# Kernel tuning notes

Hardware: AMD Instinct MI355X
Metric: run time of the kernel (lower is better)

The kernel has to match this reference:

```python
import jax, jax.numpy as jnp
import numpy as np

N_IN, N_HID, N_OUT = 128, 128, 128
BATCH = 131072

def _linear_params(key, fan_in, fan_out):
    # torch nn.Linear default init: U(-1/sqrt(fan_in), 1/sqrt(fan_in))
    kw, kb = jax.random.split(key)
    bound = 1.0 / np.sqrt(fan_in)
    W = jax.random.uniform(kw, (fan_out, fan_in), jnp.float32, -bound, bound)
    b = jax.random.uniform(kb, (fan_out,), jnp.float32, -bound, bound)
    return W, b

def setup_inputs() -> dict:
    key = jax.random.key(0)
    ks = jax.random.split(key, 6)
    x = jax.random.normal(ks[0], (BATCH, N_IN), jnp.float32)
    hidden = jnp.zeros((BATCH, N_HID), jnp.float32)
    ctx = jnp.zeros((BATCH, N_HID), jnp.float32)
    Wf, bf = _linear_params(ks[1], N_IN + N_HID, N_HID)
    Wi, bi = _linear_params(ks[2], N_IN + N_HID, N_HID)
    Wc, bc = _linear_params(ks[3], N_IN + N_HID, N_HID)
    Wo, bo = _linear_params(ks[4], N_IN + N_HID, N_HID)
    Wfc, bfc = _linear_params(ks[5], N_HID, N_OUT)
    return {"x": x, "hidden": hidden, "ctx": ctx,
            "Wf": Wf, "bf": bf, "Wi": Wi, "bi": bi,
            "Wc": Wc, "bc": bc, "Wo": Wo, "bo": bo,
            "Wfc": Wfc, "bfc": bfc}

def reference(x, hidden, ctx, Wf, bf, Wi, bi, Wc, bc, Wo, bo, Wfc, bfc):
    # cat order matches torch: (hidden, x)
    cat_input = jnp.concatenate([hidden, x], axis=1)  # [B, n_hid+n_in]
    # Stack the four gate weights into one GEMM, then split (same math).
    W4 = jnp.concatenate([Wf, Wi, Wc, Wo], axis=0)    # [4*n_hid, n_hid+n_in]
    b4 = jnp.concatenate([bf, bi, bc, bo], axis=0)
    gates = cat_input @ W4.T + b4                     # [B, 4*n_hid]
    f_lin, i_lin, c_lin, o_lin = jnp.split(gates, 4, axis=1)
    f_t = jax.nn.sigmoid(f_lin)
    i_t = jax.nn.sigmoid(i_lin)
    c_t_temp = jnp.tanh(c_lin)
    ctx_new = f_t * ctx + i_t * c_t_temp
    o_t = jax.nn.sigmoid(o_lin)
    hidden_new = o_t * jnp.tanh(ctx_new)
    out = hidden_new @ Wfc.T + bfc                    # [B, n_out]
    return (out, hidden_new, ctx_new)
```

## Files before the change

### kernel.cpp

```cpp
#include <hip/hip_runtime.h>

#define BATCH   131072
#define NHID    128
#define KDIM    256
#define BM      32
#define TPB     512
#define NBLK    256
#define NTILE   (BATCH / BM)
#define TPBLK   (NTILE / NBLK)

typedef __bf16 bf16_t;
typedef __bf16 bf16x4 __attribute__((ext_vector_type(4)));
typedef __bf16 bf16x8 __attribute__((ext_vector_type(8)));
typedef float  f32x4  __attribute__((ext_vector_type(4)));

__device__ __forceinline__ float fsigmoid(float v) {
    return __builtin_amdgcn_rcpf(1.0f + __builtin_amdgcn_exp2f(v * -1.44269504f));
}
__device__ __forceinline__ float ftanh(float v) {
    return __builtin_fmaf(-2.0f,
        __builtin_amdgcn_rcpf(1.0f + __builtin_amdgcn_exp2f(v * 2.88539008f)), 1.0f);
}

__global__ void prep_kernel(const float* __restrict__ Wf, const float* __restrict__ Wi,
                            const float* __restrict__ Wc, const float* __restrict__ Wo,
                            const float* __restrict__ bfp, const float* __restrict__ bip,
                            const float* __restrict__ bcp, const float* __restrict__ bop,
                            const float* __restrict__ Wfc,
                            bf16_t* __restrict__ W4p, float* __restrict__ b4p,
                            bf16_t* __restrict__ Wfcb)
{
    int id = blockIdx.x * 256 + threadIdx.x;
    if (id < 512 * 256) {
        int p = id >> 8, k = id & 255;
        int w = p >> 6, t = (p >> 4) & 3, c = p & 15;
        int j = w * 16 + c;
        const float* W = (t == 0) ? Wf : (t == 1) ? Wi : (t == 2) ? Wc : Wo;
        W4p[id] = (bf16_t)W[j * 256 + k];
        if (k == 0) {
            const float* bs = (t == 0) ? bfp : (t == 1) ? bip : (t == 2) ? bcp : bop;
            b4p[p] = bs[j];
        }
    } else {
        int id2 = id - 512 * 256;
        if (id2 < 128 * 128) Wfcb[id2] = (bf16_t)Wfc[id2];
    }
}

__global__ __launch_bounds__(TPB, 2) void lstm_fused(
    const float* __restrict__ x, const float* __restrict__ hidden, const float* __restrict__ ctx,
    const bf16_t* __restrict__ W4p, const float* __restrict__ b4p,
    const bf16_t* __restrict__ Wfcb, const float* __restrict__ bfc,
    float* __restrict__ out, float* __restrict__ hid_out, float* __restrict__ ctx_out)
{
    __shared__ __align__(16) char lds[2 * 16384 + 2 * 8192];

    const int tid  = threadIdx.x;
    const int lane = tid & 63;
    const int wv   = tid >> 6;
    const int l16  = lane & 15;
    const int lq   = lane >> 4;
    const int jcol = wv * 16 + l16;
    const int tile0 = blockIdx.x * TPBLK;

    const int r_s = tid >> 4;
    const int c_s = tid & 15;
    const int swzS = (r_s & 7) << 4;
    const int swzA = (l16 & 7) << 4;

    bf16x8 B1[32];
    {
        const bf16_t* Bp = W4p + (wv * 64 + l16) * 256 + lq * 8;
        #pragma unroll
        for (int gt = 0; gt < 4; ++gt)
            #pragma unroll
            for (int ks = 0; ks < 8; ++ks)
                B1[gt * 8 + ks] = *(const bf16x8*)(Bp + gt * 16 * 256 + ks * 32);
    }
    bf16x8 b2r[4];
    {
        const bf16_t* B2 = Wfcb + jcol * 128 + lq * 8;
        #pragma unroll
        for (int ks = 0; ks < 4; ++ks) b2r[ks] = *(const bf16x8*)(B2 + ks * 32);
    }
    const float bfv = b4p[wv * 64 +  0 + l16];
    const float biv = b4p[wv * 64 + 16 + l16];
    const float bcv = b4p[wv * 64 + 32 + l16];
    const float bov = b4p[wv * 64 + 48 + l16];
    const float bo2 = bfc[jcol];

    f32x4 sv0, sv1, sv2, sv3;
    float ctxr[2][4];

    {
        const int grow = tile0 * BM + r_s;
        const float* hrow = hidden + (size_t)grow * NHID + c_s * 4;
        const float* xrow = x      + (size_t)grow * NHID + c_s * 4;
        sv0 = *(const f32x4*)(hrow);
        sv1 = *(const f32x4*)(hrow + 64);
        sv2 = *(const f32x4*)(xrow);
        sv3 = *(const f32x4*)(xrow + 64);
        char* A0 = lds;
        bf16x4 p0, p1, p2, p3;
        p0[0]=(bf16_t)sv0.x; p0[1]=(bf16_t)sv0.y; p0[2]=(bf16_t)sv0.z; p0[3]=(bf16_t)sv0.w;
        p1[0]=(bf16_t)sv1.x; p1[1]=(bf16_t)sv1.y; p1[2]=(bf16_t)sv1.z; p1[3]=(bf16_t)sv1.w;
        p2[0]=(bf16_t)sv2.x; p2[1]=(bf16_t)sv2.y; p2[2]=(bf16_t)sv2.z; p2[3]=(bf16_t)sv2.w;
        p3[0]=(bf16_t)sv3.x; p3[1]=(bf16_t)sv3.y; p3[2]=(bf16_t)sv3.z; p3[3]=(bf16_t)sv3.w;
        *(bf16x4*)(A0 + r_s * 512 + ((c_s * 8 +   0) ^ swzS)) = p0;
        *(bf16x4*)(A0 + r_s * 512 + ((c_s * 8 + 128) ^ swzS)) = p1;
        *(bf16x4*)(A0 + r_s * 512 + ((c_s * 8 + 256) ^ swzS)) = p2;
        *(bf16x4*)(A0 + r_s * 512 + ((c_s * 8 + 384) ^ swzS)) = p3;
    }
    {
        const int grow = (tile0 + 1) * BM + r_s;
        const float* hrow = hidden + (size_t)grow * NHID + c_s * 4;
        const float* xrow = x      + (size_t)grow * NHID + c_s * 4;
        sv0 = *(const f32x4*)(hrow);
        sv1 = *(const f32x4*)(hrow + 64);
        sv2 = *(const f32x4*)(xrow);
        sv3 = *(const f32x4*)(xrow + 64);
    }
    {
        const float* cp = ctx + (size_t)(tile0 * BM) * NHID + jcol;
        #pragma unroll
        for (int m = 0; m < 2; ++m)
            #pragma unroll
            for (int j = 0; j < 4; ++j)
                ctxr[m][j] = cp[(m * 16 + lq * 4 + j) * NHID];
    }
    __syncthreads();

    for (int t = 0; t < TPBLK; ++t) {
        const int P = t & 1;
        const int row0 = (tile0 + t) * BM;
        char* Asb = lds + P * 16384;
        char* Hsb = lds + 32768 + P * 8192;

        f32x4 acc[2][4];
        #pragma unroll
        for (int m = 0; m < 2; ++m)
            #pragma unroll
            for (int gt = 0; gt < 4; ++gt)
                acc[m][gt] = f32x4{0.f, 0.f, 0.f, 0.f};

        #pragma unroll
        for (int ks = 0; ks < 8; ++ks) {
            const int kb = ks * 64 + lq * 16;
            bf16x8 a0 = *(const bf16x8*)(Asb + l16 * 512        + (kb ^ swzA));
            bf16x8 a1 = *(const bf16x8*)(Asb + (16 + l16) * 512 + (kb ^ swzA));
            #pragma unroll
            for (int gt = 0; gt < 4; ++gt) {
                acc[0][gt] = __builtin_amdgcn_mfma_f32_16x16x32_bf16(a0, B1[gt * 8 + ks], acc[0][gt], 0, 0, 0);
                acc[1][gt] = __builtin_amdgcn_mfma_f32_16x16x32_bf16(a1, B1[gt * 8 + ks], acc[1][gt], 0, 0, 0);
            }
        }

        float* co = ctx_out + (size_t)row0 * NHID + jcol;
        float* ho = hid_out + (size_t)row0 * NHID + jcol;
        bf16_t hnb[8];
        #pragma unroll
        for (int m = 0; m < 2; ++m) {
            #pragma unroll
            for (int j = 0; j < 4; ++j) {
                const int off = (m * 16 + lq * 4 + j) * NHID;
                const float fv = fsigmoid(acc[m][0][j] + bfv);
                const float iv = fsigmoid(acc[m][1][j] + biv);
                const float cv = ftanh(acc[m][2][j] + bcv);
                const float ov = fsigmoid(acc[m][3][j] + bov);
                const float cn = fv * ctxr[m][j] + iv * cv;
                const float hn = ov * ftanh(cn);
                co[off] = cn;
                ho[off] = hn;
                hnb[m * 4 + j] = (bf16_t)hn;
            }
        }

        {
            const int tn = (t + 1 < TPBLK) ? t + 1 : TPBLK - 1;
            const float* cp = ctx + (size_t)((tile0 + tn) * BM) * NHID + jcol;
            #pragma unroll
            for (int m = 0; m < 2; ++m)
                #pragma unroll
                for (int j = 0; j < 4; ++j)
                    ctxr[m][j] = cp[(m * 16 + lq * 4 + j) * NHID];
        }

        #pragma unroll
        for (int m = 0; m < 2; ++m)
            #pragma unroll
            for (int j = 0; j < 4; ++j) {
                const int r = m * 16 + lq * 4 + j;
                *(bf16_t*)(Hsb + r * 256 + ((jcol * 2) ^ ((r & 7) << 4))) = hnb[m * 4 + j];
            }

        {
            char* An = lds + (1 - P) * 16384;
            bf16x4 p0, p1, p2, p3;
            p0[0]=(bf16_t)sv0.x; p0[1]=(bf16_t)sv0.y; p0[2]=(bf16_t)sv0.z; p0[3]=(bf16_t)sv0.w;
            p1[0]=(bf16_t)sv1.x; p1[1]=(bf16_t)sv1.y; p1[2]=(bf16_t)sv1.z; p1[3]=(bf16_t)sv1.w;
            p2[0]=(bf16_t)sv2.x; p2[1]=(bf16_t)sv2.y; p2[2]=(bf16_t)sv2.z; p2[3]=(bf16_t)sv2.w;
            p3[0]=(bf16_t)sv3.x; p3[1]=(bf16_t)sv3.y; p3[2]=(bf16_t)sv3.z; p3[3]=(bf16_t)sv3.w;
            *(bf16x4*)(An + r_s * 512 + ((c_s * 8 +   0) ^ swzS)) = p0;
            *(bf16x4*)(An + r_s * 512 + ((c_s * 8 + 128) ^ swzS)) = p1;
            *(bf16x4*)(An + r_s * 512 + ((c_s * 8 + 256) ^ swzS)) = p2;
            *(bf16x4*)(An + r_s * 512 + ((c_s * 8 + 384) ^ swzS)) = p3;
        }

        {
            const int ts = (t + 2 < TPBLK) ? t + 2 : TPBLK - 1;
            const int grow = (tile0 + ts) * BM + r_s;
            const float* hrow = hidden + (size_t)grow * NHID + c_s * 4;
            const float* xrow = x      + (size_t)grow * NHID + c_s * 4;
            sv0 = *(const f32x4*)(hrow);
            sv1 = *(const f32x4*)(hrow + 64);
            sv2 = *(const f32x4*)(xrow);
            sv3 = *(const f32x4*)(xrow + 64);
        }

        __syncthreads();

        f32x4 acc2[2];
        acc2[0] = f32x4{0.f, 0.f, 0.f, 0.f};
        acc2[1] = f32x4{0.f, 0.f, 0.f, 0.f};
        #pragma unroll
        for (int ks = 0; ks < 4; ++ks) {
            const int kb = ks * 64 + lq * 16;
            bf16x8 a0 = *(const bf16x8*)(Hsb + l16 * 256        + (kb ^ swzA));
            bf16x8 a1 = *(const bf16x8*)(Hsb + (16 + l16) * 256 + (kb ^ swzA));
            acc2[0] = __builtin_amdgcn_mfma_f32_16x16x32_bf16(a0, b2r[ks], acc2[0], 0, 0, 0);
            acc2[1] = __builtin_amdgcn_mfma_f32_16x16x32_bf16(a1, b2r[ks], acc2[1], 0, 0, 0);
        }
        float* oo = out + (size_t)row0 * NHID + jcol;
        #pragma unroll
        for (int m = 0; m < 2; ++m)
            #pragma unroll
            for (int j = 0; j < 4; ++j)
                oo[(m * 16 + lq * 4 + j) * NHID] = acc2[m][j] + bo2;
    }
}

extern "C" void kernel_launch(void* const* d_in, const int* in_sizes, int n_in,
                              void* d_out, int out_size, void* d_ws, size_t ws_size,
                              hipStream_t stream) {
    const float* x      = (const float*)d_in[0];
    const float* hidden = (const float*)d_in[1];
    const float* ctx    = (const float*)d_in[2];
    const float* Wf     = (const float*)d_in[3];
    const float* bfp    = (const float*)d_in[4];
    const float* Wi     = (const float*)d_in[5];
    const float* bip    = (const float*)d_in[6];
    const float* Wc     = (const float*)d_in[7];
    const float* bcp    = (const float*)d_in[8];
    const float* Wo     = (const float*)d_in[9];
    const float* bop    = (const float*)d_in[10];
    const float* Wfc    = (const float*)d_in[11];
    const float* bfc    = (const float*)d_in[12];

    bf16_t* W4p  = (bf16_t*)d_ws;
    float*  b4p  = (float*)((char*)d_ws + 512 * 256 * 2);
    bf16_t* Wfcb = (bf16_t*)((char*)d_ws + 512 * 256 * 2 + 2048);

    prep_kernel<<<576, 256, 0, stream>>>(Wf, Wi, Wc, Wo, bfp, bip, bcp, bop, Wfc,
                                         W4p, b4p, Wfcb);

    float* outp = (float*)d_out;
    lstm_fused<<<NBLK, TPB, 0, stream>>>(
        x, hidden, ctx, W4p, b4p, Wfcb, bfc,
        outp,
        outp + (size_t)BATCH * NHID,
        outp + 2 * (size_t)BATCH * NHID);
}
```

Measured before the change: 122.3 us.

## Swap MFMA operands so each lane holds 4 contiguous columns for vector I/O

```diff
diff --git a/kernel.cpp b/kernel.cpp
--- a/kernel.cpp
+++ b/kernel.cpp
@@ -20,6 +20,18 @@
 __device__ __forceinline__ float ftanh(float v) {
     return __builtin_fmaf(-2.0f,
         __builtin_amdgcn_rcpf(1.0f + __builtin_amdgcn_exp2f(v * 2.88539008f)), 1.0f);
+}
+__device__ __forceinline__ f32x4 vsig(f32x4 v) {
+    f32x4 r;
+    #pragma unroll
+    for (int i = 0; i < 4; ++i) r[i] = fsigmoid(v[i]);
+    return r;
+}
+__device__ __forceinline__ f32x4 vtanh(f32x4 v) {
+    f32x4 r;
+    #pragma unroll
+    for (int i = 0; i < 4; ++i) r[i] = ftanh(v[i]);
+    return r;
 }
 
 __global__ void prep_kernel(const float* __restrict__ Wf, const float* __restrict__ Wi,
@@ -60,73 +72,61 @@
     const int wv   = tid >> 6;
     const int l16  = lane & 15;
     const int lq   = lane >> 4;
-    const int jcol = wv * 16 + l16;
     const int tile0 = blockIdx.x * TPBLK;
+    const int colb  = wv * 16 + lq * 4;
+    const int swzA  = (l16 & 7) << 4;
 
     const int r_s = tid >> 4;
     const int c_s = tid & 15;
     const int swzS = (r_s & 7) << 4;
-    const int swzA = (l16 & 7) << 4;
 
     bf16x8 B1[32];
     {
         const bf16_t* Bp = W4p + (wv * 64 + l16) * 256 + lq * 8;
         #pragma unroll
-        for (int gt = 0; gt < 4; ++gt)
+        for (int pm = 0; pm < 4; ++pm)
             #pragma unroll
             for (int ks = 0; ks < 8; ++ks)
-                B1[gt * 8 + ks] = *(const bf16x8*)(Bp + gt * 16 * 256 + ks * 32);
+                B1[pm * 8 + ks] = *(const bf16x8*)(Bp + pm * 16 * 256 + ks * 32);
     }
     bf16x8 b2r[4];
     {
-        const bf16_t* B2 = Wfcb + jcol * 128 + lq * 8;
+        const bf16_t* B2 = Wfcb + (wv * 16 + l16) * 128 + lq * 8;
         #pragma unroll
         for (int ks = 0; ks < 4; ++ks) b2r[ks] = *(const bf16x8*)(B2 + ks * 32);
     }
-    const float bfv = b4p[wv * 64 +  0 + l16];
-    const float biv = b4p[wv * 64 + 16 + l16];
-    const float bcv = b4p[wv * 64 + 32 + l16];
-    const float bov = b4p[wv * 64 + 48 + l16];
-    const float bo2 = bfc[jcol];
+    const f32x4 bf4 = *(const f32x4*)(b4p + wv * 64 +  0 + lq * 4);
+    const f32x4 bi4 = *(const f32x4*)(b4p + wv * 64 + 16 + lq * 4);
+    const f32x4 bc4 = *(const f32x4*)(b4p + wv * 64 + 32 + lq * 4);
+    const f32x4 bo4 = *(const f32x4*)(b4p + wv * 64 + 48 + lq * 4);
+    const f32x4 bfc4 = *(const f32x4*)(bfc + colb);
 
     f32x4 sv0, sv1, sv2, sv3;
-    float ctxr[2][4];
+    f32x4 ctxA[2], ctxB[2];
 
     {
         const int grow = tile0 * BM + r_s;
         const float* hrow = hidden + (size_t)grow * NHID + c_s * 4;
         const float* xrow = x      + (size_t)grow * NHID + c_s * 4;
-        sv0 = *(const f32x4*)(hrow);
-        sv1 = *(const f32x4*)(hrow + 64);
-        sv2 = *(const f32x4*)(xrow);
-        sv3 = *(const f32x4*)(xrow + 64);
+        f32x4 t0 = *(const f32x4*)(hrow);
+        f32x4 t1 = *(const f32x4*)(hrow + 64);
+        f32x4 t2 = *(const f32x4*)(xrow);
+        f32x4 t3 = *(const f32x4*)(xrow + 64);
         char* A0 = lds;
         bf16x4 p0, p1, p2, p3;
-        p0[0]=(bf16_t)sv0.x; p0[1]=(bf16_t)sv0.y; p0[2]=(bf16_t)sv0.z; p0[3]=(bf16_t)sv0.w;
-        p1[0]=(bf16_t)sv1.x; p1[1]=(bf16_t)sv1.y; p1[2]=(bf16_t)sv1.z; p1[3]=(bf16_t)sv1.w;
-        p2[0]=(bf16_t)sv2.x; p2[1]=(bf16_t)sv2.y; p2[2]=(bf16_t)sv2.z; p2[3]=(bf16_t)sv2.w;
-        p3[0]=(bf16_t)sv3.x; p3[1]=(bf16_t)sv3.y; p3[2]=(bf16_t)sv3.z; p3[3]=(bf16_t)sv3.w;
+        p0[0]=(bf16_t)t0.x; p0[1]=(bf16_t)t0.y; p0[2]=(bf16_t)t0.z; p0[3]=(bf16_t)t0.w;
+        p1[0]=(bf16_t)t1.x; p1[1]=(bf16_t)t1.y; p1[2]=(bf16_t)t1.z; p1[3]=(bf16_t)t1.w;
+        p2[0]=(bf16_t)t2.x; p2[1]=(bf16_t)t2.y; p2[2]=(bf16_t)t2.z; p2[3]=(bf16_t)t2.w;
+        p3[0]=(bf16_t)t3.x; p3[1]=(bf16_t)t3.y; p3[2]=(bf16_t)t3.z; p3[3]=(bf16_t)t3.w;
         *(bf16x4*)(A0 + r_s * 512 + ((c_s * 8 +   0) ^ swzS)) = p0;
         *(bf16x4*)(A0 + r_s * 512 + ((c_s * 8 + 128) ^ swzS)) = p1;
         *(bf16x4*)(A0 + r_s * 512 + ((c_s * 8 + 256) ^ swzS)) = p2;
         *(bf16x4*)(A0 + r_s * 512 + ((c_s * 8 + 384) ^ swzS)) = p3;
     }
     {
-        const int grow = (tile0 + 1) * BM + r_s;
-        const float* hrow = hidden + (size_t)grow * NHID + c_s * 4;
-        const float* xrow = x      + (size_t)grow * NHID + c_s * 4;
-        sv0 = *(const f32x4*)(hrow);
-        sv1 = *(const f32x4*)(hrow + 64);
-        sv2 = *(const f32x4*)(xrow);
-        sv3 = *(const f32x4*)(xrow + 64);
-    }
-    {
-        const float* cp = ctx + (size_t)(tile0 * BM) * NHID + jcol;
-        #pragma unroll
-        for (int m = 0; m < 2; ++m)
-            #pragma unroll
-            for (int j = 0; j < 4; ++j)
-                ctxr[m][j] = cp[(m * 16 + lq * 4 + j) * NHID];
+        const float* cp = ctx + (size_t)(tile0 * BM) * NHID + colb;
+        ctxA[0] = *(const f32x4*)(cp + (size_t)l16 * NHID);
+        ctxA[1] = *(const f32x4*)(cp + (size_t)(16 + l16) * NHID);
     }
     __syncthreads();
 
@@ -136,62 +136,57 @@
         char* Asb = lds + P * 16384;
         char* Hsb = lds + 32768 + P * 8192;
 
-        f32x4 acc[2][4];
-        #pragma unroll
-        for (int m = 0; m < 2; ++m)
-            #pragma unroll
-            for (int gt = 0; gt < 4; ++gt)
-                acc[m][gt] = f32x4{0.f, 0.f, 0.f, 0.f};
-
+        {
+            const int tn = (t + 1 < TPBLK) ? t + 1 : TPBLK - 1;
+            const int grow = (tile0 + tn) * BM + r_s;
+            const float* hrow = hidden + (size_t)grow * NHID + c_s * 4;
+            const float* xrow = x      + (size_t)grow * NHID + c_s * 4;
+            sv0 = *(const f32x4*)(hrow);
+            sv1 = *(const f32x4*)(hrow + 64);
+            sv2 = *(const f32x4*)(xrow);
+            sv3 = *(const f32x4*)(xrow + 64);
+            const float* cp = ctx + (size_t)((tile0 + tn) * BM) * NHID + colb;
+            ctxB[0] = *(const f32x4*)(cp + (size_t)l16 * NHID);
+            ctxB[1] = *(const f32x4*)(cp + (size_t)(16 + l16) * NHID);
+        }
+
+        f32x4 acc[4][2];
+        #pragma unroll
+        for (int pm = 0; pm < 4; ++pm) {
+            acc[pm][0] = f32x4{0.f, 0.f, 0.f, 0.f};
+            acc[pm][1] = f32x4{0.f, 0.f, 0.f, 0.f};
+        }
         #pragma unroll
         for (int ks = 0; ks < 8; ++ks) {
             const int kb = ks * 64 + lq * 16;
             bf16x8 a0 = *(const bf16x8*)(Asb + l16 * 512        + (kb ^ swzA));
             bf16x8 a1 = *(const bf16x8*)(Asb + (16 + l16) * 512 + (kb ^ swzA));
             #pragma unroll
-            for (int gt = 0; gt < 4; ++gt) {
-                acc[0][gt] = __builtin_amdgcn_mfma_f32_16x16x32_bf16(a0, B1[gt * 8 + ks], acc[0][gt], 0, 0, 0);
-                acc[1][gt] = __builtin_amdgcn_mfma_f32_16x16x32_bf16(a1, B1[gt * 8 + ks], acc[1][gt], 0, 0, 0);
+            for (int pm = 0; pm < 4; ++pm) {
+                acc[pm][0] = __builtin_amdgcn_mfma_f32_16x16x32_bf16(B1[pm * 8 + ks], a0, acc[pm][0], 0, 0, 0);
+                acc[pm][1] = __builtin_amdgcn_mfma_f32_16x16x32_bf16(B1[pm * 8 + ks], a1, acc[pm][1], 0, 0, 0);
             }
         }
 
-        float* co = ctx_out + (size_t)row0 * NHID + jcol;
-        float* ho = hid_out + (size_t)row0 * NHID + jcol;
-        bf16_t hnb[8];
-        #pragma unroll
-        for (int m = 0; m < 2; ++m) {
-            #pragma unroll
-            for (int j = 0; j < 4; ++j) {
-                const int off = (m * 16 + lq * 4 + j) * NHID;
-                const float fv = fsigmoid(acc[m][0][j] + bfv);
-                const float iv = fsigmoid(acc[m][1][j] + biv);
-                const float cv = ftanh(acc[m][2][j] + bcv);
-                const float ov = fsigmoid(acc[m][3][j] + bov);
-                const float cn = fv * ctxr[m][j] + iv * cv;
-                const float hn = ov * ftanh(cn);
-                co[off] = cn;
-                ho[off] = hn;
-                hnb[m * 4 + j] = (bf16_t)hn;
-            }
-        }
-
-        {
-            const int tn = (t + 1 < TPBLK) ? t + 1 : TPBLK - 1;
-            const float* cp = ctx + (size_t)((tile0 + tn) * BM) * NHID + jcol;
-            #pragma unroll
-            for (int m = 0; m < 2; ++m)
-                #pragma unroll
-                for (int j = 0; j < 4; ++j)
-                    ctxr[m][j] = cp[(m * 16 + lq * 4 + j) * NHID];
-        }
-
-        #pragma unroll
-        for (int m = 0; m < 2; ++m)
-            #pragma unroll
-            for (int j = 0; j < 4; ++j) {
-                const int r = m * 16 + lq * 4 + j;
-                *(bf16_t*)(Hsb + r * 256 + ((jcol * 2) ^ ((r & 7) << 4))) = hnb[m * 4 + j];
-            }
+        #pragma unroll
+        for (int bn = 0; bn < 2; ++bn) {
+            const size_t grow = (size_t)(row0 + bn * 16 + l16) * NHID + colb;
+            const f32x4 fv = vsig(acc[0][bn] + bf4);
+            const f32x4 iv = vsig(acc[1][bn] + bi4);
+            const f32x4 cv = vtanh(acc[2][bn] + bc4);
+            const f32x4 ov = vsig(acc[3][bn] + bo4);
+            const f32x4 cn = fv * ctxA[bn] + iv * cv;
+            const f32x4 hn = ov * vtanh(cn);
+            *(f32x4*)(ctx_out + grow) = cn;
+            *(f32x4*)(hid_out + grow) = hn;
+            bf16x4 hb;
+            hb[0] = (bf16_t)hn.x; hb[1] = (bf16_t)hn.y;
+            hb[2] = (bf16_t)hn.z; hb[3] = (bf16_t)hn.w;
+            const int rh = bn * 16 + l16;
+            *(bf16x4*)(Hsb + rh * 256 + ((wv * 32 + lq * 8) ^ ((rh & 7) << 4))) = hb;
+        }
+        ctxA[0] = ctxB[0];
+        ctxA[1] = ctxB[1];
 
         {
             char* An = lds + (1 - P) * 16384;
@@ -206,17 +201,6 @@
             *(bf16x4*)(An + r_s * 512 + ((c_s * 8 + 384) ^ swzS)) = p3;
         }
 
-        {
-            const int ts = (t + 2 < TPBLK) ? t + 2 : TPBLK - 1;
-            const int grow = (tile0 + ts) * BM + r_s;
-            const float* hrow = hidden + (size_t)grow * NHID + c_s * 4;
-            const float* xrow = x      + (size_t)grow * NHID + c_s * 4;
-            sv0 = *(const f32x4*)(hrow);
-            sv1 = *(const f32x4*)(hrow + 64);
-            sv2 = *(const f32x4*)(xrow);
-            sv3 = *(const f32x4*)(xrow + 64);
-        }
-
         __syncthreads();
 
         f32x4 acc2[2];
@@ -225,17 +209,16 @@
         #pragma unroll
         for (int ks = 0; ks < 4; ++ks) {
             const int kb = ks * 64 + lq * 16;
-            bf16x8 a0 = *(const bf16x8*)(Hsb + l16 * 256        + (kb ^ swzA));
-            bf16x8 a1 = *(const bf16x8*)(Hsb + (16 + l16) * 256 + (kb ^ swzA));
-            acc2[0] = __builtin_amdgcn_mfma_f32_16x16x32_bf16(a0, b2r[ks], acc2[0], 0, 0, 0);
-            acc2[1] = __builtin_amdgcn_mfma_f32_16x16x32_bf16(a1, b2r[ks], acc2[1], 0, 0, 0);
-        }
-        float* oo = out + (size_t)row0 * NHID + jcol;
-        #pragma unroll
-        for (int m = 0; m < 2; ++m)
-            #pragma unroll
-            for (int j = 0; j < 4; ++j)
-                oo[(m * 16 + lq * 4 + j) * NHID] = acc2[m][j] + bo2;
+            bf16x8 h0 = *(const bf16x8*)(Hsb + l16 * 256        + (kb ^ swzA));
+            bf16x8 h1 = *(const bf16x8*)(Hsb + (16 + l16) * 256 + (kb ^ swzA));
+            acc2[0] = __builtin_amdgcn_mfma_f32_16x16x32_bf16(b2r[ks], h0, acc2[0], 0, 0, 0);
+            acc2[1] = __builtin_amdgcn_mfma_f32_16x16x32_bf16(b2r[ks], h1, acc2[1], 0, 0, 0);
+        }
+        #pragma unroll
+        for (int bn = 0; bn < 2; ++bn) {
+            const size_t grow = (size_t)(row0 + bn * 16 + l16) * NHID + colb;
+            *(f32x4*)(out + grow) = acc2[bn] + bfc4;
+        }
     }
 }
 
```

Result: faster. 117.0 us (-4.3%).
